# Kernel optimization log

Hardware: AMD Instinct MI355X
Metric: run time of the kernel (lower is better)

## Reference

```python
import jax, jax.numpy as jnp
import numpy as np

LAGS = 2
SLOPE = 0.2  # LeakyReLU negative slope


def _mlp(z, W0, b0, W1, b1, W2, b2, W3, b3):
    # z: [N, E+1] -> [N, 1]; 3 hidden LeakyReLU layers + linear output (MLP2, num_layers=3)
    h = jax.nn.leaky_relu(z @ W0.T + b0, SLOPE)
    h = jax.nn.leaky_relu(h @ W1.T + b1, SLOPE)
    h = jax.nn.leaky_relu(h @ W2.T + b2, SLOPE)
    return h @ W3.T + b3


def setup_inputs() -> dict:
    key = jax.random.key(0)
    ks = jax.random.split(key, 11)
    B, T, L, E, H = 64, 1000, 8, 16, 64  # batch, lags+length, latent_size, embedding_dim, hidden_dim
    x = jax.random.normal(ks[0], (B, T, L), dtype=jnp.float32)
    embeddings = jax.random.normal(ks[1], (1, T, E), dtype=jnp.float32)
    def w(k, shape, fan_in):
        return jax.random.normal(k, shape, dtype=jnp.float32) / np.float32(np.sqrt(fan_in))
    gW0 = w(ks[2], (L, H, E + 1), E + 1)
    gb0 = jax.random.normal(ks[3], (L, H), dtype=jnp.float32) * 0.05
    gW1 = w(ks[4], (L, H, H), H)
    gb1 = jax.random.normal(ks[5], (L, H), dtype=jnp.float32) * 0.05
    gW2 = w(ks[6], (L, H, H), H)
    gb2 = jax.random.normal(ks[7], (L, H), dtype=jnp.float32) * 0.05
    gW3 = w(ks[8], (L, 1, H), H)
    gb3 = jax.random.normal(ks[9], (L, 1), dtype=jnp.float32) * 0.05
    return {"x": x, "embeddings": embeddings,
            "gW0": gW0, "gb0": gb0, "gW1": gW1, "gb1": gb1,
            "gW2": gW2, "gb2": gb2, "gW3": gW3, "gb3": gb3}


def reference(x, embeddings, gW0, gb0, gW1, gb1, gW2, gb2, gW3, gb3):
    B, T, L = x.shape
    E = embeddings.shape[-1]
    length = T - LAGS
    N = B * length
    # last element of each length-(lags+1) sliding window is x[:, LAGS:]
    x_t = x[:, LAGS:, :].reshape(N, L)  # [N, L]
    emb = jnp.broadcast_to(embeddings[:, -length:], (B, length, E)).reshape(N, E)  # [N, E]
    # per-latent inputs: [L, N, E+1] (embedding shared, last coord = x_t[:, i])
    inp = jnp.concatenate(
        [jnp.broadcast_to(emb[None], (L, N, E)), x_t.T[:, :, None]], axis=-1)

    def per_latent(params, z):
        W0, b0, W1, b1, W2, b2, W3, b3 = params
        f = lambda zz: _mlp(zz, W0, b0, W1, b1, W2, b2, W3, b3)
        # jacfwd(f)(z)[:, -1] == jvp with unit tangent on last input coordinate
        tan = jnp.zeros_like(z).at[:, -1].set(1.0)
        out, dout = jax.jvp(f, (z,), (tan,))
        return out[:, 0], dout[:, 0]

    res, J = jax.vmap(per_latent)((gW0, gb0, gW1, gb1, gW2, gb2, gW3, gb3), inp)  # [L, N] each
    residuals = res.T.reshape(B, length, L)
    log_abs_det_jacobian = jnp.sum(jnp.log(jnp.abs(J)), axis=0).reshape(B, length)
    return residuals, log_abs_det_jacobian
```

## Files before the change

### kernel.cpp

```cpp
#include <hip/hip_runtime.h>

typedef unsigned short u16;
typedef float f32x4 __attribute__((ext_vector_type(4)));
typedef __fp16 f16x2 __attribute__((ext_vector_type(2)));
typedef __fp16 half8 __attribute__((ext_vector_type(8)));
typedef unsigned int uint2v __attribute__((ext_vector_type(2)));
typedef unsigned int uint4v __attribute__((ext_vector_type(4)));

#define STRW 72
#define STRU 36
#define LENT 998
#define NSAMP 63872
#define TILE_U16 4608
#define INVS 4.8828125e-4f

#define LDSFENCE() asm volatile("s_waitcnt lgkmcnt(0)" ::: "memory")

static __device__ __forceinline__ uint2v split2s(float x, float y) {
    f16x2 h = __builtin_amdgcn_cvt_pkrtz(x, y);
    f16x2 l = __builtin_amdgcn_cvt_pkrtz((x - (float)h[0]) * 2048.f,
                                         (y - (float)h[1]) * 2048.f);
    uint2v r;
    r[0] = __builtin_bit_cast(unsigned int, h);
    r[1] = __builtin_bit_cast(unsigned int, l);
    return r;
}
static __device__ __forceinline__ void split8s(f32x4 A, f32x4 B,
                                               uint4v* hi, uint4v* lo) {
    uint2v r0 = split2s(A[0], A[1]);
    uint2v r1 = split2s(A[2], A[3]);
    uint2v r2 = split2s(B[0], B[1]);
    uint2v r3 = split2s(B[2], B[3]);
    uint4v h, l;
    h[0] = r0[0]; l[0] = r0[1];
    h[1] = r1[0]; l[1] = r1[1];
    h[2] = r2[0]; l[2] = r2[1];
    h[3] = r3[0]; l[3] = r3[1];
    *hi = h; *lo = l;
}

__global__ __launch_bounds__(256, 4) void mlp_h2(
    const float* __restrict__ xp,  const float* __restrict__ embp,
    const float* __restrict__ gW0p, const float* __restrict__ gb0p,
    const float* __restrict__ gW1p, const float* __restrict__ gb1p,
    const float* __restrict__ gW2p, const float* __restrict__ gb2p,
    const float* __restrict__ gW3p, const float* __restrict__ gb3p,
    float* __restrict__ out)
{
    __shared__ u16 sWa[TILE_U16], sWb[TILE_U16];
    __shared__ unsigned int scrH[4][16 * STRU];
    __shared__ unsigned int scrD[4][16 * STRU];
    __shared__ float sb1[64], sb2[64], sw3[64], sw0c[64], sE0[64], semb[16];

    const int tid = threadIdx.x;
    const int wave = tid >> 6, lane = tid & 63;
    const int q = lane >> 4, s = lane & 15;
    const int t = blockIdx.x;
    const int bsmp = wave * 16 + s;
    const f32x4 zf = {0.f, 0.f, 0.f, 0.f};

    if (tid < 16) semb[tid] = embp[(t + 2) * 16 + tid];
    float ldAcc = 0.f;

    const int srow = tid >> 2, scol = (tid & 3) * 16;

    for (int l = 0; l < 8; ++l) {
        __syncthreads();
        {
            const f32x4* g = (const f32x4*)(gW1p + (size_t)l * 4096) + tid * 4;
#pragma unroll
            for (int h = 0; h < 2; ++h) {
                uint4v hi, lo;
                split8s(g[h * 2], g[h * 2 + 1], &hi, &lo);
                const int o = srow * STRW + scol + h * 8;
                *(uint4v*)&sWa[o] = hi;
                *(uint4v*)&sWb[o] = lo;
            }
        }
        if (tid < 64) {
            const float* r = gW0p + (size_t)(l * 64 + tid) * 17;
            float acc = gb0p[l * 64 + tid];
#pragma unroll
            for (int e = 0; e < 16; e++) acc = fmaf(r[e], semb[e], acc);
            sE0[tid]  = acc;
            sw0c[tid] = r[16];
            sb1[tid]  = gb1p[l * 64 + tid];
            sb2[tid]  = gb2p[l * 64 + tid];
            sw3[tid]  = gW3p[l * 64 + tid];
        }
        __syncthreads();

        const float b3v = gb3p[l];
        const float xv = xp[(size_t)(bsmp * 1000 + t + 2) * 8 + l];

        half8 H0a[2], H0b[2], D0a[2], D0b[2];
#pragma unroll
        for (int kc = 0; kc < 2; ++kc) {
            f32x4 eA = *(const f32x4*)&sE0[kc * 32 + q * 8];
            f32x4 eB = *(const f32x4*)&sE0[kc * 32 + q * 8 + 4];
            f32x4 wA = *(const f32x4*)&sw0c[kc * 32 + q * 8];
            f32x4 wB = *(const f32x4*)&sw0c[kc * 32 + q * 8 + 4];
            float hv[8], dv[8];
#pragma unroll
            for (int i = 0; i < 8; ++i) {
                float w  = (i < 4) ? wA[i] : wB[i - 4];
                float e0 = (i < 4) ? eA[i] : eB[i - 4];
                float p  = fmaf(w, xv, e0);
                hv[i] = fmaxf(p, 0.2f * p);
                dv[i] = (p >= 0.f ? 1.f : 0.2f) * w;
            }
            uint4v Ha, Hb, Da, Db;
#pragma unroll
            for (int d2 = 0; d2 < 4; ++d2) {
                uint2v rh = split2s(hv[2 * d2], hv[2 * d2 + 1]);
                uint2v rd = split2s(dv[2 * d2], dv[2 * d2 + 1]);
                Ha[d2] = rh[0]; Hb[d2] = rh[1];
                Da[d2] = rd[0]; Db[d2] = rd[1];
            }
            H0a[kc] = __builtin_bit_cast(half8, Ha);
            H0b[kc] = __builtin_bit_cast(half8, Hb);
            D0a[kc] = __builtin_bit_cast(half8, Da);
            D0b[kc] = __builtin_bit_cast(half8, Db);
        }

        f32x4 aA[4], aX[4], tA[4], tX[4];
#pragma unroll
        for (int mb = 0; mb < 4; ++mb) { aA[mb] = zf; aX[mb] = zf; tA[mb] = zf; tX[mb] = zf; }
#pragma unroll
        for (int kc = 0; kc < 2; ++kc) {
#pragma unroll
            for (int mb = 0; mb < 4; ++mb) {
                const int wo = (mb * 16 + s) * STRW + kc * 32 + q * 8;
                half8 wa = __builtin_bit_cast(half8, *(const uint4v*)&sWa[wo]);
                half8 wb = __builtin_bit_cast(half8, *(const uint4v*)&sWb[wo]);
                aA[mb] = __builtin_amdgcn_mfma_f32_16x16x32_f16(wa, H0a[kc], aA[mb], 0, 0, 0);
                aX[mb] = __builtin_amdgcn_mfma_f32_16x16x32_f16(wa, H0b[kc], aX[mb], 0, 0, 0);
                aX[mb] = __builtin_amdgcn_mfma_f32_16x16x32_f16(wb, H0a[kc], aX[mb], 0, 0, 0);
                tA[mb] = __builtin_amdgcn_mfma_f32_16x16x32_f16(wa, D0a[kc], tA[mb], 0, 0, 0);
                tX[mb] = __builtin_amdgcn_mfma_f32_16x16x32_f16(wa, D0b[kc], tX[mb], 0, 0, 0);
                tX[mb] = __builtin_amdgcn_mfma_f32_16x16x32_f16(wb, D0a[kc], tX[mb], 0, 0, 0);
            }
        }

        uint2v hpH[4], hpL[4], dpH[4], dpL[4];
#pragma unroll
        for (int mb = 0; mb < 4; ++mb) {
            f32x4 b1v = *(const f32x4*)&sb1[mb * 16 + q * 4];
            float hv[4], dv[4];
#pragma unroll
            for (int i = 0; i < 4; ++i) {
                float p  = fmaf(aX[mb][i], INVS, aA[mb][i]) + b1v[i];
                float dt = fmaf(tX[mb][i], INVS, tA[mb][i]);
                hv[i] = fmaxf(p, 0.2f * p);
                dv[i] = (p >= 0.f ? 1.f : 0.2f) * dt;
            }
            uint2v r0 = split2s(hv[0], hv[1]);
            uint2v r1 = split2s(hv[2], hv[3]);
            uint2v r2 = split2s(dv[0], dv[1]);
            uint2v r3 = split2s(dv[2], dv[3]);
            hpH[mb][0] = r0[0]; hpL[mb][0] = r0[1];
            hpH[mb][1] = r1[0]; hpL[mb][1] = r1[1];
            dpH[mb][0] = r2[0]; dpL[mb][0] = r2[1];
            dpH[mb][1] = r3[0]; dpL[mb][1] = r3[1];
        }
        unsigned int* mH = scrH[wave];
        unsigned int* mD = scrD[wave];
        half8 H1a[2], H1b[2], D1a[2], D1b[2];
#pragma unroll
        for (int mb = 0; mb < 4; ++mb) {
            *(uint2v*)&mH[s * STRU + mb * 8 + q * 2] = hpH[mb];
            *(uint2v*)&mD[s * STRU + mb * 8 + q * 2] = dpH[mb];
        }
        LDSFENCE();
#pragma unroll
        for (int kc = 0; kc < 2; ++kc) {
            H1a[kc] = __builtin_bit_cast(half8, *(const uint4v*)&mH[s * STRU + kc * 16 + q * 4]);
            D1a[kc] = __builtin_bit_cast(half8, *(const uint4v*)&mD[s * STRU + kc * 16 + q * 4]);
        }
        LDSFENCE();
#pragma unroll
        for (int mb = 0; mb < 4; ++mb) {
            *(uint2v*)&mH[s * STRU + mb * 8 + q * 2] = hpL[mb];
            *(uint2v*)&mD[s * STRU + mb * 8 + q * 2] = dpL[mb];
        }
        LDSFENCE();
#pragma unroll
        for (int kc = 0; kc < 2; ++kc) {
            H1b[kc] = __builtin_bit_cast(half8, *(const uint4v*)&mH[s * STRU + kc * 16 + q * 4]);
            D1b[kc] = __builtin_bit_cast(half8, *(const uint4v*)&mD[s * STRU + kc * 16 + q * 4]);
        }

        __syncthreads();
        {
            const f32x4* g = (const f32x4*)(gW2p + (size_t)l * 4096) + tid * 4;
#pragma unroll
            for (int h = 0; h < 2; ++h) {
                uint4v hi, lo;
                split8s(g[h * 2], g[h * 2 + 1], &hi, &lo);
                const int o = srow * STRW + scol + h * 8;
                *(uint4v*)&sWa[o] = hi;
                *(uint4v*)&sWb[o] = lo;
            }
        }
        __syncthreads();

#pragma unroll
        for (int mb = 0; mb < 4; ++mb) { aA[mb] = zf; aX[mb] = zf; tA[mb] = zf; tX[mb] = zf; }
#pragma unroll
        for (int kc = 0; kc < 2; ++kc) {
#pragma unroll
            for (int mb = 0; mb < 4; ++mb) {
                const int wo = (mb * 16 + s) * STRW + kc * 32 + q * 8;
                half8 wa = __builtin_bit_cast(half8, *(const uint4v*)&sWa[wo]);
                half8 wb = __builtin_bit_cast(half8, *(const uint4v*)&sWb[wo]);
                aA[mb] = __builtin_amdgcn_mfma_f32_16x16x32_f16(wa, H1a[kc], aA[mb], 0, 0, 0);
                aX[mb] = __builtin_amdgcn_mfma_f32_16x16x32_f16(wa, H1b[kc], aX[mb], 0, 0, 0);
                aX[mb] = __builtin_amdgcn_mfma_f32_16x16x32_f16(wb, H1a[kc], aX[mb], 0, 0, 0);
                tA[mb] = __builtin_amdgcn_mfma_f32_16x16x32_f16(wa, D1a[kc], tA[mb], 0, 0, 0);
                tX[mb] = __builtin_amdgcn_mfma_f32_16x16x32_f16(wa, D1b[kc], tX[mb], 0, 0, 0);
                tX[mb] = __builtin_amdgcn_mfma_f32_16x16x32_f16(wb, D1a[kc], tX[mb], 0, 0, 0);
            }
        }

        float rs = 0.f, js = 0.f;
#pragma unroll
        for (int mb = 0; mb < 4; ++mb) {
            f32x4 b2v = *(const f32x4*)&sb2[mb * 16 + q * 4];
            f32x4 w3v = *(const f32x4*)&sw3[mb * 16 + q * 4];
#pragma unroll
            for (int i = 0; i < 4; ++i) {
                float p  = fmaf(aX[mb][i], INVS, aA[mb][i]) + b2v[i];
                float dt = fmaf(tX[mb][i], INVS, tA[mb][i]);
                float h = fmaxf(p, 0.2f * p);
                float d = (p >= 0.f ? 1.f : 0.2f) * dt;
                rs = fmaf(w3v[i], h, rs);
                js = fmaf(w3v[i], d, js);
            }
        }
        rs += __shfl_xor(rs, 16, 64); rs += __shfl_xor(rs, 32, 64);
        js += __shfl_xor(js, 16, 64); js += __shfl_xor(js, 32, 64);
        if (lane < 16)
            out[(size_t)(bsmp * LENT + t) * 8 + l] = rs + b3v;
        ldAcc += __logf(fabsf(js));
    }

    if (lane < 16)
        out[(size_t)NSAMP * 8 + (size_t)bsmp * LENT + t] = ldAcc;
}

extern "C" void kernel_launch(void* const* d_in, const int* in_sizes, int n_in,
                              void* d_out, int out_size, void* d_ws, size_t ws_size,
                              hipStream_t stream) {
    (void)in_sizes; (void)n_in; (void)out_size; (void)d_ws; (void)ws_size;
    mlp_h2<<<dim3(LENT), 256, 0, stream>>>(
        (const float*)d_in[0], (const float*)d_in[1],
        (const float*)d_in[2], (const float*)d_in[3],
        (const float*)d_in[4], (const float*)d_in[5],
        (const float*)d_in[6], (const float*)d_in[7],
        (const float*)d_in[8], (const float*)d_in[9],
        (float*)d_out);
}
```

Measured before the change: 141.7 us.

## Precompute split-fp16 weight images in workspace and DMA them into LDS

Adds a prep kernel that converts W1/W2 into hi/lo fp16 LDS-layout images once, and also precomputes the per-timestep embedding projection E0 and per-latent vectors in workspace. The main kernel then copies these images with global_load_lds instead of having every block redo the fp32 load and split conversion. This removes redundant per-block conversion ALU work and register traffic. In exchange it adds a second launch, extra workspace traffic, and a full vmcnt wait before the barrier. It falls back to the old path if the workspace is missing or too small.

```diff
diff --git a/kernel.cpp b/kernel.cpp
--- a/kernel.cpp
+++ b/kernel.cpp
@@ -1,6 +1,7 @@
 #include <hip/hip_runtime.h>
 
 typedef unsigned short u16;
+typedef unsigned int u32;
 typedef float f32x4 __attribute__((ext_vector_type(4)));
 typedef __fp16 f16x2 __attribute__((ext_vector_type(2)));
 typedef __fp16 half8 __attribute__((ext_vector_type(8)));
@@ -14,7 +15,18 @@
 #define TILE_U16 4608
 #define INVS 4.8828125e-4f
 
+#define IMG_BYTES 18432
+#define WS_VEC_OFF (16 * IMG_BYTES)
+#define WS_E0_OFF  (WS_VEC_OFF + 8 * 256 * 4)
+#define WS_NEED    ((size_t)WS_E0_OFF + (size_t)LENT * 512 * 4)
+
 #define LDSFENCE() asm volatile("s_waitcnt lgkmcnt(0)" ::: "memory")
+
+static __device__ __forceinline__ void gll16(const void* g, void* l) {
+    __builtin_amdgcn_global_load_lds(
+        (const __attribute__((address_space(1))) void*)g,
+        (__attribute__((address_space(3))) void*)l, 16, 0, 0);
+}
 
 static __device__ __forceinline__ uint2v split2s(float x, float y) {
     f16x2 h = __builtin_amdgcn_cvt_pkrtz(x, y);
@@ -39,18 +51,82 @@
     *hi = h; *lo = l;
 }
 
+__global__ __launch_bounds__(256) void prep_ws(
+    const float* __restrict__ gW0p, const float* __restrict__ gb0p,
+    const float* __restrict__ gW1p, const float* __restrict__ gb1p,
+    const float* __restrict__ gW2p, const float* __restrict__ gb2p,
+    const float* __restrict__ gW3p, const float* __restrict__ embp,
+    char* __restrict__ ws)
+{
+    const int tid = threadIdx.x;
+    const int bid = blockIdx.x;
+    __shared__ float se[16];
+
+    if (bid < 16) {
+        const int layer = bid >> 3, l = bid & 7;
+        const float* src = (layer ? gW2p : gW1p) + (size_t)l * 4096;
+        u16* img = (u16*)(ws + (size_t)bid * IMG_BYTES);
+        const int srow = tid >> 2, scol = (tid & 3) * 16;
+        const f32x4* g = (const f32x4*)src + tid * 4;
+#pragma unroll
+        for (int h = 0; h < 2; ++h) {
+            uint4v hi, lo;
+            split8s(g[h * 2], g[h * 2 + 1], &hi, &lo);
+            const int o = srow * STRW + scol + h * 8;
+            *(uint4v*)&img[o] = hi;
+            *(uint4v*)&img[TILE_U16 + o] = lo;
+        }
+        if ((tid & 3) == 3) {
+            const uint4v z = {0, 0, 0, 0};
+            *(uint4v*)&img[srow * STRW + 64] = z;
+            *(uint4v*)&img[TILE_U16 + srow * STRW + 64] = z;
+        }
+        if (layer == 0 && tid < 64) {
+            float* vec = (float*)(ws + WS_VEC_OFF) + l * 256;
+            const float* r = gW0p + (size_t)(l * 64 + tid) * 17;
+            vec[tid]       = r[16];
+            vec[64 + tid]  = gb1p[l * 64 + tid];
+            vec[128 + tid] = gb2p[l * 64 + tid];
+            vec[192 + tid] = gW3p[l * 64 + tid];
+        }
+    } else {
+        const int t = bid - 16;
+        if (tid < 16) se[tid] = embp[(t + 2) * 16 + tid];
+        __syncthreads();
+        float* eo = (float*)(ws + WS_E0_OFF) + (size_t)t * 512;
+#pragma unroll
+        for (int p = 0; p < 2; ++p) {
+            const int idx = tid + p * 256;
+            const int l = idx >> 6, row = idx & 63;
+            const float* r = gW0p + (size_t)(l * 64 + row) * 17;
+            float acc = gb0p[l * 64 + row];
+#pragma unroll
+            for (int e = 0; e < 16; ++e) acc = fmaf(r[e], se[e], acc);
+            eo[idx] = acc;
+        }
+    }
+}
+
 __global__ __launch_bounds__(256, 4) void mlp_h2(
     const float* __restrict__ xp,  const float* __restrict__ embp,
     const float* __restrict__ gW0p, const float* __restrict__ gb0p,
     const float* __restrict__ gW1p, const float* __restrict__ gb1p,
     const float* __restrict__ gW2p, const float* __restrict__ gb2p,
     const float* __restrict__ gW3p, const float* __restrict__ gb3p,
-    float* __restrict__ out)
+    float* __restrict__ out, const char* __restrict__ wsr, int use_ws)
 {
-    __shared__ u16 sWa[TILE_U16], sWb[TILE_U16];
+    __shared__ u16 sW2[2][TILE_U16];
     __shared__ unsigned int scrH[4][16 * STRU];
     __shared__ unsigned int scrD[4][16 * STRU];
-    __shared__ float sb1[64], sb2[64], sw3[64], sw0c[64], sE0[64], semb[16];
+    __shared__ float sVec[256];
+    __shared__ float sE0[64], semb[16];
+
+    u16* const sWa = sW2[0];
+    u16* const sWb = sW2[1];
+    float* const sw0c = sVec;
+    float* const sb1  = sVec + 64;
+    float* const sb2  = sVec + 128;
+    float* const sw3  = sVec + 192;
 
     const int tid = threadIdx.x;
     const int wave = tid >> 6, lane = tid & 63;
@@ -59,34 +135,48 @@
     const int bsmp = wave * 16 + s;
     const f32x4 zf = {0.f, 0.f, 0.f, 0.f};
 
-    if (tid < 16) semb[tid] = embp[(t + 2) * 16 + tid];
+    if (!use_ws && tid < 16) semb[tid] = embp[(t + 2) * 16 + tid];
     float ldAcc = 0.f;
 
     const int srow = tid >> 2, scol = (tid & 3) * 16;
 
     for (int l = 0; l < 8; ++l) {
         __syncthreads();
-        {
-            const f32x4* g = (const f32x4*)(gW1p + (size_t)l * 4096) + tid * 4;
-#pragma unroll
-            for (int h = 0; h < 2; ++h) {
-                uint4v hi, lo;
-                split8s(g[h * 2], g[h * 2 + 1], &hi, &lo);
-                const int o = srow * STRW + scol + h * 8;
-                *(uint4v*)&sWa[o] = hi;
-                *(uint4v*)&sWb[o] = lo;
-            }
-        }
-        if (tid < 64) {
-            const float* r = gW0p + (size_t)(l * 64 + tid) * 17;
-            float acc = gb0p[l * 64 + tid];
-#pragma unroll
-            for (int e = 0; e < 16; e++) acc = fmaf(r[e], semb[e], acc);
-            sE0[tid]  = acc;
-            sw0c[tid] = r[16];
-            sb1[tid]  = gb1p[l * 64 + tid];
-            sb2[tid]  = gb2p[l * 64 + tid];
-            sw3[tid]  = gW3p[l * 64 + tid];
+        if (use_ws) {
+            const char* img = wsr + (size_t)l * IMG_BYTES;
+#pragma unroll
+            for (int c = 0; c < 4; ++c)
+                gll16(img + c * 4096 + tid * 16, (char*)sW2 + c * 4096 + wave * 1024);
+            if (tid < 128)
+                gll16(img + 16384 + tid * 16, (char*)sW2 + 16384 + wave * 1024);
+            sVec[tid] = *(const float*)(wsr + WS_VEC_OFF + (size_t)(l * 256 + tid) * 4);
+            if (tid < 64)
+                sE0[tid] = *(const float*)(wsr + WS_E0_OFF +
+                                           ((size_t)t * 512 + l * 64 + tid) * 4);
+            asm volatile("s_waitcnt vmcnt(0)" ::: "memory");
+        } else {
+            {
+                const f32x4* g = (const f32x4*)(gW1p + (size_t)l * 4096) + tid * 4;
+#pragma unroll
+                for (int h = 0; h < 2; ++h) {
+                    uint4v hi, lo;
+                    split8s(g[h * 2], g[h * 2 + 1], &hi, &lo);
+                    const int o = srow * STRW + scol + h * 8;
+                    *(uint4v*)&sWa[o] = hi;
+                    *(uint4v*)&sWb[o] = lo;
+                }
+            }
+            if (tid < 64) {
+                const float* r = gW0p + (size_t)(l * 64 + tid) * 17;
+                float acc = gb0p[l * 64 + tid];
+#pragma unroll
+                for (int e = 0; e < 16; e++) acc = fmaf(r[e], semb[e], acc);
+                sE0[tid]  = acc;
+                sw0c[tid] = r[16];
+                sb1[tid]  = gb1p[l * 64 + tid];
+                sb2[tid]  = gb2p[l * 64 + tid];
+                sw3[tid]  = gW3p[l * 64 + tid];
+            }
         }
         __syncthreads();
 
@@ -191,7 +281,15 @@
         }
 
         __syncthreads();
-        {
+        if (use_ws) {
+            const char* img = wsr + (size_t)(8 + l) * IMG_BYTES;
+#pragma unroll
+            for (int c = 0; c < 4; ++c)
+                gll16(img + c * 4096 + tid * 16, (char*)sW2 + c * 4096 + wave * 1024);
+            if (tid < 128)
+                gll16(img + 16384 + tid * 16, (char*)sW2 + 16384 + wave * 1024);
+            asm volatile("s_waitcnt vmcnt(0)" ::: "memory");
+        } else {
             const f32x4* g = (const f32x4*)(gW2p + (size_t)l * 4096) + tid * 4;
 #pragma unroll
             for (int h = 0; h < 2; ++h) {
@@ -251,12 +349,21 @@
 extern "C" void kernel_launch(void* const* d_in, const int* in_sizes, int n_in,
                               void* d_out, int out_size, void* d_ws, size_t ws_size,
                               hipStream_t stream) {
-    (void)in_sizes; (void)n_in; (void)out_size; (void)d_ws; (void)ws_size;
+    (void)in_sizes; (void)n_in; (void)out_size;
+    const int use_ws = (d_ws != nullptr && ws_size >= WS_NEED) ? 1 : 0;
+    if (use_ws) {
+        prep_ws<<<dim3(16 + LENT), 256, 0, stream>>>(
+            (const float*)d_in[2], (const float*)d_in[3],
+            (const float*)d_in[4], (const float*)d_in[5],
+            (const float*)d_in[6], (const float*)d_in[7],
+            (const float*)d_in[8], (const float*)d_in[1],
+            (char*)d_ws);
+    }
     mlp_h2<<<dim3(LENT), 256, 0, stream>>>(
         (const float*)d_in[0], (const float*)d_in[1],
         (const float*)d_in[2], (const float*)d_in[3],
         (const float*)d_in[4], (const float*)d_in[5],
         (const float*)d_in[6], (const float*)d_in[7],
         (const float*)d_in[8], (const float*)d_in[9],
-        (float*)d_out);
-}
+        (float*)d_out, (const char*)d_ws, use_ws);
+}
```

New measurement: 140.9 us. No clear change (-0.6%).
